# Kernel optimization log

Measured on AMD Instinct MI355X. Metric: run time of the kernel, lower is better.

## Reference

```python
import jax, jax.numpy as jnp
import numpy as np

HEADS = 16
DIM = 1024
D_K = DIM // HEADS
SEQ = 2048


def setup_inputs() -> dict:
    key = jax.random.key(0)
    ks = jax.random.split(key, 11)
    s = 1.0 / np.sqrt(DIM).astype(np.float32)
    return {
        "q": jax.random.normal(ks[0], (SEQ, DIM), jnp.float32),
        "k": jax.random.normal(ks[1], (SEQ, DIM), jnp.float32),
        "v": jax.random.normal(ks[2], (SEQ, DIM), jnp.float32),
        "Wq": jax.random.normal(ks[3], (DIM, DIM), jnp.float32) * s,
        "bq": jax.random.normal(ks[4], (DIM,), jnp.float32) * 0.01,
        "Wk": jax.random.normal(ks[5], (DIM, DIM), jnp.float32) * s,
        "bk": jax.random.normal(ks[6], (DIM,), jnp.float32) * 0.01,
        "Wv": jax.random.normal(ks[7], (DIM, DIM), jnp.float32) * s,
        "bv": jax.random.normal(ks[8], (DIM,), jnp.float32) * 0.01,
        "Wo": jax.random.normal(ks[9], (DIM, DIM), jnp.float32) * s,
        "bo": jax.random.normal(ks[10], (DIM,), jnp.float32) * 0.01,
    }


def reference(q, k, v, Wq, bq, Wk, bk, Wv, bv, Wo, bo):
    S = q.shape[0]
    # torch Linear: x @ W.T + b; view to (1, S, H, d_k) then transpose to (1, H, S, d_k)
    def proj(x, W, b):
        return (x @ W.T + b).reshape(1, S, HEADS, D_K).transpose(0, 2, 1, 3)

    qh = proj(q, Wq, bq)  # (1, H, S, d)
    kh = proj(k, Wk, bk)
    vh = proj(v, Wv, bv)

    scale = 1.0 / np.sqrt(D_K).astype(np.float32)
    scores = jnp.einsum("bhqd,bhkd->bhqk", qh, kh) * scale  # (1, H, S, S)
    # NOTE: source applies softmax over dim=1 == the HEADS axis (faithful quirk)
    attn = jax.nn.softmax(scores, axis=1)
    ctx = jnp.einsum("bhqk,bhkd->bhqd", attn, vh)  # (1, H, S, d)
    concat = ctx.transpose(0, 2, 1, 3).reshape(1, S, DIM)
    return concat @ Wo.T + bo
```

## Files before the change

kernel.cpp:

```cpp
#include <hip/hip_runtime.h>
#include <hip/hip_fp16.h>


typedef _Float16 f16;
typedef _Float16 f16x4 __attribute__((ext_vector_type(4)));
typedef _Float16 f16x8 __attribute__((ext_vector_type(8)));
typedef float    f32x4 __attribute__((ext_vector_type(4)));

#define S_LEN 2048
#define DIM   1024
#define NH    16
#define DK    64
#define EXP2K 0.1803368801111244f

#define MFMA(a, b, c) __builtin_amdgcn_mfma_f32_16x16x32_f16(a, b, c, 0, 0, 0)

#define VM_WAIT0   asm volatile("s_waitcnt vmcnt(0)" ::: "memory")
#define WG_BARRIER asm volatile("s_barrier" ::: "memory")

typedef __attribute__((address_space(1))) void g_void;
typedef __attribute__((address_space(3))) void l_void;

static __device__ __forceinline__ void gload_lds16(const void* g, void* l) {
  __builtin_amdgcn_global_load_lds((g_void*)g, (l_void*)l, 16, 0, 0);
}

static __device__ __forceinline__ float exp_s(float s) {
  return __builtin_amdgcn_exp2f(s * EXP2K);
}

__global__ __launch_bounds__(256) void cvt_all(
    const float* __restrict__ q, const float* __restrict__ k, const float* __restrict__ v,
    const float* __restrict__ Wq, const float* __restrict__ Wk, const float* __restrict__ Wv,
    const float* __restrict__ Wo, f16* __restrict__ qh, f16* __restrict__ kh,
    f16* __restrict__ vh, f16* __restrict__ wqh, f16* __restrict__ wkh,
    f16* __restrict__ wvh, f16* __restrict__ woh) {
  const size_t M = 1048576;
  const int seg = blockIdx.y;
  const float* src;
  f16* dst;
  switch (seg) {
    case 0: src = q;      dst = qh;      break;
    case 1: src = q + M;  dst = qh + M;  break;
    case 2: src = k;      dst = kh;      break;
    case 3: src = k + M;  dst = kh + M;  break;
    case 4: src = v;      dst = vh;      break;
    case 5: src = v + M;  dst = vh + M;  break;
    case 6: src = Wq;     dst = wqh;     break;
    case 7: src = Wk;     dst = wkh;     break;
    case 8: src = Wv;     dst = wvh;     break;
    default: src = Wo;    dst = woh;     break;
  }
  int i = blockIdx.x * 256 + threadIdx.x;
  float4 vv = ((const float4*)src)[i];
  f16x4 o = {(f16)vv.x, (f16)vv.y, (f16)vv.z, (f16)vv.w};
  ((f16x4*)dst)[i] = o;
}

__global__ __launch_bounds__(256) void cvt_f32_f16(const float* __restrict__ src,
                                                   f16* __restrict__ dst, int n4) {
  int i = blockIdx.x * 256 + threadIdx.x;
  if (i < n4) {
    float4 v = ((const float4*)src)[i];
    f16x4 o = {(f16)v.x, (f16)v.y, (f16)v.z, (f16)v.w};
    ((f16x4*)dst)[i] = o;
  }
}

static __device__ __forceinline__ void gemm32_core(const f16* __restrict__ X,
                                                   const f16* __restrict__ W,
                                                   int k0, int k1, int bm, int bn,
                                                   f16* As, f16* Bs,
                                                   f32x4 (&acc)[4][2]) {
  const int tid = threadIdx.x;
  const int wv = tid >> 6;
  const int lane = tid & 63;
  const int qd = lane >> 4;
  const int l16 = lane & 15;
  const int wm = (wv & 1) * 64;
  const int wn = (wv >> 1) * 32;
  const int lr4 = lane >> 2, lc4 = lane & 3;

  const f16* gA = X + (size_t)(bm + wv * 32 + lr4) * DIM + k0 + lc4 * 8;
  const f16* gB = W + (size_t)(bn + wv * 16 + lr4) * DIM + k0 + lc4 * 8;
  const int np = (k1 - k0) >> 5;

  gload_lds16(gA, As + (wv * 32) * 32);
  gload_lds16(gA + 16 * DIM, As + (wv * 32 + 16) * 32);
  gload_lds16(gB, Bs + (wv * 16) * 32);

#pragma unroll 2
  for (int t = 0; t < np; t++) {
    const int buf = t & 1;
    VM_WAIT0;
    WG_BARRIER;
    if (t + 1 < np) {
      const f16* gA1 = gA + (t + 1) * 32;
      const f16* gB1 = gB + (t + 1) * 32;
      f16* dA = As + (buf ^ 1) * (128 * 32);
      f16* dB = Bs + (buf ^ 1) * (64 * 32);
      gload_lds16(gA1, dA + (wv * 32) * 32);
      gload_lds16(gA1 + 16 * DIM, dA + (wv * 32 + 16) * 32);
      gload_lds16(gB1, dB + (wv * 16) * 32);
    }
    const f16* A = As + buf * (128 * 32);
    const f16* B = Bs + buf * (64 * 32);
    f16x8 bf[2];
#pragma unroll
    for (int ni = 0; ni < 2; ni++)
      bf[ni] = *(const f16x8*)&B[(wn + ni * 16 + l16) * 32 + qd * 8];
#pragma unroll
    for (int mi = 0; mi < 4; mi++) {
      f16x8 af = *(const f16x8*)&A[(wm + mi * 16 + l16) * 32 + qd * 8];
#pragma unroll
      for (int ni = 0; ni < 2; ni++)
        acc[mi][ni] = MFMA(af, bf[ni], acc[mi][ni]);
    }
  }
}

__global__ __launch_bounds__(256) void gemm_qkv(
    const f16* __restrict__ X0, const f16* __restrict__ X1, const f16* __restrict__ X2,
    const f16* __restrict__ W0, const f16* __restrict__ W1, const f16* __restrict__ W2,
    const float* __restrict__ b0, const float* __restrict__ b1, const float* __restrict__ b2,
    f16* __restrict__ o0, f16* __restrict__ o1, f16* __restrict__ o2) {
  __shared__ __align__(16) f16 As[2 * 128 * 32];
  __shared__ __align__(16) f16 Bs[2 * 64 * 32];
  const int z = blockIdx.z;
  const f16* X = z == 0 ? X0 : z == 1 ? X1 : X2;
  const f16* W = z == 0 ? W0 : z == 1 ? W1 : W2;
  const float* bias = z == 0 ? b0 : z == 1 ? b1 : b2;
  f16* outh = z == 0 ? o0 : z == 1 ? o1 : o2;

  const int bm = blockIdx.y * 128, bn = blockIdx.x * 64;
  f32x4 acc[4][2];
#pragma unroll
  for (int a = 0; a < 4; a++)
#pragma unroll
    for (int b = 0; b < 2; b++) acc[a][b] = (f32x4){0.f, 0.f, 0.f, 0.f};

  gemm32_core(X, W, 0, DIM, bm, bn, As, Bs, acc);

  const int tid = threadIdx.x;
  const int wv = tid >> 6, lane = tid & 63;
  const int qd = lane >> 4, l16 = lane & 15;
  const int wm = (wv & 1) * 64, wn = (wv >> 1) * 32;
#pragma unroll
  for (int mi = 0; mi < 4; mi++) {
#pragma unroll
    for (int ni = 0; ni < 2; ni++) {
      const int gm = bm + wm + mi * 16 + qd * 4;
      const int gn = bn + wn + ni * 16 + l16;
      const float bs = bias[gn];
      if (z == 2) {
        f16x4 o = {(f16)(acc[mi][ni][0] + bs), (f16)(acc[mi][ni][1] + bs),
                   (f16)(acc[mi][ni][2] + bs), (f16)(acc[mi][ni][3] + bs)};
        *(f16x4*)&outh[(size_t)gn * S_LEN + gm] = o;
      } else {
#pragma unroll
        for (int r = 0; r < 4; r++)
          outh[(size_t)(gm + r) * DIM + gn] = (f16)(acc[mi][ni][r] + bs);
      }
    }
  }
}

__global__ __launch_bounds__(256) void gemm_out(const f16* __restrict__ X,
                                                const f16* __restrict__ W,
                                                const float* __restrict__ bias,
                                                float* __restrict__ outf) {
  __shared__ __align__(16) f16 As[2 * 128 * 32];
  __shared__ __align__(16) f16 Bs[2 * 64 * 32];
  const int z = blockIdx.z;
  const int bm = blockIdx.y * 128, bn = blockIdx.x * 64;
  f32x4 acc[4][2];
#pragma unroll
  for (int a = 0; a < 4; a++)
#pragma unroll
    for (int b = 0; b < 2; b++) acc[a][b] = (f32x4){0.f, 0.f, 0.f, 0.f};

  gemm32_core(X, W, z * (DIM / 2), (z + 1) * (DIM / 2), bm, bn, As, Bs, acc);

  const int tid = threadIdx.x;
  const int wv = tid >> 6, lane = tid & 63;
  const int qd = lane >> 4, l16 = lane & 15;
  const int wm = (wv & 1) * 64, wn = (wv >> 1) * 32;
#pragma unroll
  for (int mi = 0; mi < 4; mi++) {
#pragma unroll
    for (int ni = 0; ni < 2; ni++) {
      const int gm = bm + wm + mi * 16 + qd * 4;
      const int gn = bn + wn + ni * 16 + l16;
      const float bs = z == 0 ? bias[gn] : 0.f;
#pragma unroll
      for (int r = 0; r < 4; r++)
        atomicAdd(&outf[(size_t)(gm + r) * DIM + gn], acc[mi][ni][r] + bs);
    }
  }
}

__global__ __launch_bounds__(256) void attn_denom(const f16* __restrict__ Qp,
                                                  const f16* __restrict__ Kp,
                                                  f16* __restrict__ IDn) {
  __shared__ __align__(16) f16 Qs[2][2][64 * 32];
  __shared__ __align__(16) f16 Ks[2][2][64 * 32];
  const int tid = threadIdx.x;
  const int wv = tid >> 6;
  const int lane = tid & 63;
  const int qd = lane >> 4;
  const int l16 = lane & 15;
  const int wm = (wv & 1) * 32, wn = (wv >> 1) * 32;
  const int bi = blockIdx.y * 64, bj = blockIdx.x * 64;
  const int lr4 = lane >> 2, lc4 = lane & 3;
  const int kkw = wv & 1;
  const int q0 = (wv >> 1) * 2;

  f32x4 dsum[2][2];
#pragma unroll
  for (int a = 0; a < 2; a++)
#pragma unroll
    for (int b = 0; b < 2; b++) dsum[a][b] = (f32x4){0.f, 0.f, 0.f, 0.f};

  {
    const f16* gq = Qp + (size_t)(bi + q0 * 16 + lr4) * DIM + kkw * 32 + lc4 * 8;
    const f16* gk = Kp + (size_t)(bj + q0 * 16 + lr4) * DIM + kkw * 32 + lc4 * 8;
#pragma unroll
    for (int t = 0; t < 2; t++) {
      gload_lds16(gq + (size_t)t * 16 * DIM, &Qs[0][kkw][(q0 + t) * 16 * 32]);
      gload_lds16(gk + (size_t)t * 16 * DIM, &Ks[0][kkw][(q0 + t) * 16 * 32]);
    }
  }

#pragma unroll 2
  for (int h = 0; h < NH; h++) {
    const int buf = h & 1;
    VM_WAIT0;
    WG_BARRIER;
    if (h + 1 < NH) {
      const f16* gq = Qp + (size_t)(bi + q0 * 16 + lr4) * DIM + (h + 1) * DK + kkw * 32 + lc4 * 8;
      const f16* gk = Kp + (size_t)(bj + q0 * 16 + lr4) * DIM + (h + 1) * DK + kkw * 32 + lc4 * 8;
#pragma unroll
      for (int t = 0; t < 2; t++) {
        gload_lds16(gq + (size_t)t * 16 * DIM, &Qs[buf ^ 1][kkw][(q0 + t) * 16 * 32]);
        gload_lds16(gk + (size_t)t * 16 * DIM, &Ks[buf ^ 1][kkw][(q0 + t) * 16 * 32]);
      }
    }

#pragma unroll
    for (int mi = 0; mi < 2; mi++) {
      f16x8 af0 = *(const f16x8*)&Qs[buf][0][(wm + mi * 16 + l16) * 32 + qd * 8];
      f16x8 af1 = *(const f16x8*)&Qs[buf][1][(wm + mi * 16 + l16) * 32 + qd * 8];
#pragma unroll
      for (int ni = 0; ni < 2; ni++) {
        f16x8 bf0 = *(const f16x8*)&Ks[buf][0][(wn + ni * 16 + l16) * 32 + qd * 8];
        f16x8 bf1 = *(const f16x8*)&Ks[buf][1][(wn + ni * 16 + l16) * 32 + qd * 8];
        f32x4 s = {0.f, 0.f, 0.f, 0.f};
        s = MFMA(af0, bf0, s);
        s = MFMA(af1, bf1, s);
#pragma unroll
        for (int r = 0; r < 4; r++) dsum[mi][ni][r] += exp_s(s[r]);
      }
    }
  }
#pragma unroll
  for (int mi = 0; mi < 2; mi++)
#pragma unroll
    for (int ni = 0; ni < 2; ni++)
#pragma unroll
      for (int r = 0; r < 4; r++) {
        const int gi = bi + wm + mi * 16 + qd * 4 + r;
        const int gj = bj + wn + ni * 16 + l16;
        IDn[(size_t)gi * S_LEN + gj] = (f16)(1.f / dsum[mi][ni][r]);
      }
}

__global__ __launch_bounds__(256, 4) void attn_ctx(const f16* __restrict__ Qp,
                                                   const f16* __restrict__ Kp,
                                                   const f16* __restrict__ Vt,
                                                   const f16* __restrict__ IDn,
                                                   float* __restrict__ Cp) {
  __shared__ __align__(16) f16 Ks[2][2][32 * 32];
  __shared__ __align__(16) f16 Vs[2][64 * 32];
  __shared__ __align__(16) f16 Pl[4][32 * 40];
  const int tid = threadIdx.x;
  const int wv = tid >> 6;
  const int lane = tid & 63;
  const int qd = lane >> 4;
  const int l16 = lane & 15;
  const int h = blockIdx.y;
  const int i0 = blockIdx.x * 128;
  const int iw = i0 + wv * 32;
  const int jb = blockIdx.z * 512;
  const int lr4 = lane >> 2, lc4 = lane & 3;
  const int kkw = wv & 1;
  const int rhw = wv >> 1;
  f16* pl = Pl[wv];

  f16x8 aq[2][2];
#pragma unroll
  for (int mi = 0; mi < 2; mi++)
#pragma unroll
    for (int kk = 0; kk < 2; kk++)
      aq[mi][kk] = *(const f16x8*)(Qp + (size_t)(iw + mi * 16 + l16) * DIM +
                                   h * DK + kk * 32 + qd * 8);

  f32x4 acc[2][4];
#pragma unroll
  for (int a = 0; a < 2; a++)
#pragma unroll
    for (int b = 0; b < 4; b++) acc[a][b] = (f32x4){0.f, 0.f, 0.f, 0.f};

  f16x8 idn[2][2];

  {
    const int j0 = jb;
    gload_lds16(Kp + (size_t)(j0 + rhw * 16 + lr4) * DIM + h * DK + kkw * 32 + lc4 * 8,
                &Ks[0][kkw][(rhw * 16) * 32]);
    gload_lds16(Vt + (size_t)(h * DK + wv * 16 + lr4) * S_LEN + j0 + lc4 * 8,
                &Vs[0][(wv * 16) * 32]);
#pragma unroll
    for (int mi = 0; mi < 2; mi++)
      idn[0][mi] = *(const f16x8*)(IDn + (size_t)(iw + mi * 16 + l16) * S_LEN + j0 + qd * 8);
  }

#pragma unroll 2
  for (int jt = 0; jt < 16; jt++) {
    const int buf = jt & 1;
    VM_WAIT0;
    WG_BARRIER;

    if (jt + 1 < 16) {
      const int j1 = jb + (jt + 1) * 32;
      gload_lds16(Kp + (size_t)(j1 + rhw * 16 + lr4) * DIM + h * DK + kkw * 32 + lc4 * 8,
                  &Ks[buf ^ 1][kkw][(rhw * 16) * 32]);
      gload_lds16(Vt + (size_t)(h * DK + wv * 16 + lr4) * S_LEN + j1 + lc4 * 8,
                  &Vs[buf ^ 1][(wv * 16) * 32]);
#pragma unroll
      for (int mi = 0; mi < 2; mi++)
        idn[buf ^ 1][mi] =
            *(const f16x8*)(IDn + (size_t)(iw + mi * 16 + l16) * S_LEN + j1 + qd * 8);
    }

    f16x8 bk[2][2];
#pragma unroll
    for (int ni = 0; ni < 2; ni++)
#pragma unroll
      for (int kk = 0; kk < 2; kk++)
        bk[ni][kk] = *(const f16x8*)&Ks[buf][kk][(ni * 16 + l16) * 32 + qd * 8];
#pragma unroll
    for (int mi = 0; mi < 2; mi++)
#pragma unroll
      for (int ni = 0; ni < 2; ni++) {
        f32x4 s = {0.f, 0.f, 0.f, 0.f};
        s = MFMA(aq[mi][0], bk[ni][0], s);
        s = MFMA(aq[mi][1], bk[ni][1], s);
#pragma unroll
        for (int r = 0; r < 4; r++)
          pl[(mi * 16 + qd * 4 + r) * 40 + ni * 16 + l16] = (f16)exp_s(s[r]);
      }

    f16x8 bv[4];
#pragma unroll
    for (int nd = 0; nd < 4; nd++)
      bv[nd] = *(const f16x8*)&Vs[buf][(nd * 16 + l16) * 32 + qd * 8];
#pragma unroll
    for (int mi = 0; mi < 2; mi++) {
      f16x8 ef = *(const f16x8*)&pl[(mi * 16 + l16) * 40 + qd * 8];
      f16x8 p = ef * idn[buf][mi];
#pragma unroll
      for (int nd = 0; nd < 4; nd++)
        acc[mi][nd] = MFMA(p, bv[nd], acc[mi][nd]);
    }
  }

#pragma unroll
  for (int mi = 0; mi < 2; mi++)
#pragma unroll
    for (int nd = 0; nd < 4; nd++)
#pragma unroll
      for (int r = 0; r < 4; r++)
        atomicAdd(&Cp[(size_t)(iw + mi * 16 + qd * 4 + r) * DIM + h * DK + nd * 16 + l16],
                  acc[mi][nd][r]);
}

extern "C" void kernel_launch(void* const* d_in, const int* in_sizes, int n_in,
                              void* d_out, int out_size, void* d_ws, size_t ws_size,
                              hipStream_t stream) {
  const float* q  = (const float*)d_in[0];
  const float* k  = (const float*)d_in[1];
  const float* v  = (const float*)d_in[2];
  const float* Wq = (const float*)d_in[3];
  const float* bq = (const float*)d_in[4];
  const float* Wk = (const float*)d_in[5];
  const float* bk = (const float*)d_in[6];
  const float* Wv = (const float*)d_in[7];
  const float* bv = (const float*)d_in[8];
  const float* Wo = (const float*)d_in[9];
  const float* bo = (const float*)d_in[10];
  float* out = (float*)d_out;

  f16* w = (f16*)d_ws;
  f16* qh  = w;
  f16* kh  = qh + (size_t)S_LEN * DIM;
  f16* vh  = kh + (size_t)S_LEN * DIM;
  f16* wqh = vh + (size_t)S_LEN * DIM;
  f16* wkh = wqh + (size_t)DIM * DIM;
  f16* wvh = wkh + (size_t)DIM * DIM;
  f16* woh = wvh + (size_t)DIM * DIM;
  f16* Qp  = woh + (size_t)DIM * DIM;
  f16* Kp  = Qp + (size_t)S_LEN * DIM;
  f16* Vt  = Kp + (size_t)S_LEN * DIM;
  f16* IDn = qh;
  float* Cp = (float*)vh;
  f16* Ct  = qh;

  dim3 b256(256);
  cvt_all<<<dim3(1024, 10), b256, 0, stream>>>(q, k, v, Wq, Wk, Wv, Wo,
                                               qh, kh, vh, wqh, wkh, wvh, woh);

  gemm_qkv<<<dim3(DIM / 64, S_LEN / 128, 3), b256, 0, stream>>>(
      qh, kh, vh, wqh, wkh, wvh, bq, bk, bv, Qp, Kp, Vt);

  hipMemsetAsync(Cp, 0, (size_t)S_LEN * DIM * sizeof(float), stream);
  hipMemsetAsync(out, 0, (size_t)S_LEN * DIM * sizeof(float), stream);

  attn_denom<<<dim3(S_LEN / 64, S_LEN / 64), b256, 0, stream>>>(Qp, Kp, IDn);
  attn_ctx<<<dim3(S_LEN / 128, NH, 4), b256, 0, stream>>>(Qp, Kp, Vt, IDn, Cp);

  const int nqkv4 = S_LEN * DIM / 4;
  cvt_f32_f16<<<nqkv4 / 256, b256, 0, stream>>>(Cp, Ct, nqkv4);

  gemm_out<<<dim3(DIM / 64, S_LEN / 128, 2), b256, 0, stream>>>(Ct, woh, bo, out);
}
```

Baseline: 229.3 us.

## Keep softmax probabilities in registers via transposed MFMA, swizzle V in LDS, split keys 8 ways

The attention-context kernel now computes scores with swapped MFMA operands (K as A, Q as B), so each lane's score outputs already sit in the A-operand layout for the P·V MFMA. This removes the per-wave LDS round trip for the exp'd probabilities, and the Pl shared buffer is dropped. V tiles are loaded into LDS with an XOR swizzle and read back as two f16x4 halves, aiming to cut bank conflicts. The key range per block is halved and the grid z doubled, with launch bounds raised to 5. The cost is more fp32 atomicAdd traffic into Cp and more blocks.

```diff
diff --git a/kernel.cpp b/kernel.cpp
--- a/kernel.cpp
+++ b/kernel.cpp
@@ -274,14 +274,13 @@
       }
 }
 
-__global__ __launch_bounds__(256, 4) void attn_ctx(const f16* __restrict__ Qp,
+__global__ __launch_bounds__(256, 5) void attn_ctx(const f16* __restrict__ Qp,
                                                    const f16* __restrict__ Kp,
                                                    const f16* __restrict__ Vt,
                                                    const f16* __restrict__ IDn,
                                                    float* __restrict__ Cp) {
   __shared__ __align__(16) f16 Ks[2][2][32 * 32];
   __shared__ __align__(16) f16 Vs[2][64 * 32];
-  __shared__ __align__(16) f16 Pl[4][32 * 40];
   const int tid = threadIdx.x;
   const int wv = tid >> 6;
   const int lane = tid & 63;
@@ -290,11 +289,10 @@
   const int h = blockIdx.y;
   const int i0 = blockIdx.x * 128;
   const int iw = i0 + wv * 32;
-  const int jb = blockIdx.z * 512;
+  const int jb = blockIdx.z * 256;
   const int lr4 = lane >> 2, lc4 = lane & 3;
   const int kkw = wv & 1;
   const int rhw = wv >> 1;
-  f16* pl = Pl[wv];
 
   f16x8 aq[2][2];
 #pragma unroll
@@ -310,35 +308,43 @@
 #pragma unroll
     for (int b = 0; b < 4; b++) acc[a][b] = (f32x4){0.f, 0.f, 0.f, 0.f};
 
-  f16x8 idn[2][2];
+  f16x4 idn[2][2][2];
+
+  const int vswz = (lc4 ^ ((lr4 >> 1) & 3)) * 8;
 
   {
     const int j0 = jb;
     gload_lds16(Kp + (size_t)(j0 + rhw * 16 + lr4) * DIM + h * DK + kkw * 32 + lc4 * 8,
                 &Ks[0][kkw][(rhw * 16) * 32]);
-    gload_lds16(Vt + (size_t)(h * DK + wv * 16 + lr4) * S_LEN + j0 + lc4 * 8,
+    gload_lds16(Vt + (size_t)(h * DK + wv * 16 + lr4) * S_LEN + j0 + vswz,
                 &Vs[0][(wv * 16) * 32]);
 #pragma unroll
     for (int mi = 0; mi < 2; mi++)
-      idn[0][mi] = *(const f16x8*)(IDn + (size_t)(iw + mi * 16 + l16) * S_LEN + j0 + qd * 8);
+#pragma unroll
+      for (int ni = 0; ni < 2; ni++)
+        idn[0][mi][ni] = *(const f16x4*)(IDn + (size_t)(iw + mi * 16 + l16) * S_LEN +
+                                         j0 + ni * 16 + qd * 4);
   }
 
 #pragma unroll 2
-  for (int jt = 0; jt < 16; jt++) {
+  for (int jt = 0; jt < 8; jt++) {
     const int buf = jt & 1;
     VM_WAIT0;
     WG_BARRIER;
 
-    if (jt + 1 < 16) {
+    if (jt + 1 < 8) {
       const int j1 = jb + (jt + 1) * 32;
       gload_lds16(Kp + (size_t)(j1 + rhw * 16 + lr4) * DIM + h * DK + kkw * 32 + lc4 * 8,
                   &Ks[buf ^ 1][kkw][(rhw * 16) * 32]);
-      gload_lds16(Vt + (size_t)(h * DK + wv * 16 + lr4) * S_LEN + j1 + lc4 * 8,
+      gload_lds16(Vt + (size_t)(h * DK + wv * 16 + lr4) * S_LEN + j1 + vswz,
                   &Vs[buf ^ 1][(wv * 16) * 32]);
 #pragma unroll
       for (int mi = 0; mi < 2; mi++)
-        idn[buf ^ 1][mi] =
-            *(const f16x8*)(IDn + (size_t)(iw + mi * 16 + l16) * S_LEN + j1 + qd * 8);
+#pragma unroll
+        for (int ni = 0; ni < 2; ni++)
+          idn[buf ^ 1][mi][ni] =
+              *(const f16x4*)(IDn + (size_t)(iw + mi * 16 + l16) * S_LEN +
+                              j1 + ni * 16 + qd * 4);
     }
 
     f16x8 bk[2][2];
@@ -347,30 +353,43 @@
 #pragma unroll
       for (int kk = 0; kk < 2; kk++)
         bk[ni][kk] = *(const f16x8*)&Ks[buf][kk][(ni * 16 + l16) * 32 + qd * 8];
+
+    f16x8 pa[2];
+#pragma unroll
+    for (int mi = 0; mi < 2; mi++) {
+      f32x4 st0 = {0.f, 0.f, 0.f, 0.f};
+      f32x4 st1 = {0.f, 0.f, 0.f, 0.f};
+      st0 = MFMA(bk[0][0], aq[mi][0], st0);
+      st0 = MFMA(bk[0][1], aq[mi][1], st0);
+      st1 = MFMA(bk[1][0], aq[mi][0], st1);
+      st1 = MFMA(bk[1][1], aq[mi][1], st1);
+      const f16x4 i0v = idn[buf][mi][0];
+      const f16x4 i1v = idn[buf][mi][1];
+      f16x8 p;
+#pragma unroll
+      for (int r = 0; r < 4; r++) p[r] = (f16)(exp_s(st0[r]) * (float)i0v[r]);
+#pragma unroll
+      for (int r = 0; r < 4; r++) p[4 + r] = (f16)(exp_s(st1[r]) * (float)i1v[r]);
+      pa[mi] = p;
+    }
+
+    const int xsw = (l16 >> 1) & 3;
+    const int q04 = (qd & 1) * 4;
+    const int sq = qd >> 1;
+    f16x8 bv[4];
+#pragma unroll
+    for (int nd = 0; nd < 4; nd++) {
+      const f16* vb = &Vs[buf][(nd * 16 + l16) * 32];
+      f16x4 lo = *(const f16x4*)&vb[((sq ^ xsw) * 8) + q04];
+      f16x4 hi = *(const f16x4*)&vb[(((2 + sq) ^ xsw) * 8) + q04];
+      bv[nd] = __builtin_shufflevector(lo, hi, 0, 1, 2, 3, 4, 5, 6, 7);
+    }
+
 #pragma unroll
     for (int mi = 0; mi < 2; mi++)
 #pragma unroll
-      for (int ni = 0; ni < 2; ni++) {
-        f32x4 s = {0.f, 0.f, 0.f, 0.f};
-        s = MFMA(aq[mi][0], bk[ni][0], s);
-        s = MFMA(aq[mi][1], bk[ni][1], s);
-#pragma unroll
-        for (int r = 0; r < 4; r++)
-          pl[(mi * 16 + qd * 4 + r) * 40 + ni * 16 + l16] = (f16)exp_s(s[r]);
-      }
-
-    f16x8 bv[4];
-#pragma unroll
-    for (int nd = 0; nd < 4; nd++)
-      bv[nd] = *(const f16x8*)&Vs[buf][(nd * 16 + l16) * 32 + qd * 8];
-#pragma unroll
-    for (int mi = 0; mi < 2; mi++) {
-      f16x8 ef = *(const f16x8*)&pl[(mi * 16 + l16) * 40 + qd * 8];
-      f16x8 p = ef * idn[buf][mi];
-#pragma unroll
       for (int nd = 0; nd < 4; nd++)
-        acc[mi][nd] = MFMA(p, bv[nd], acc[mi][nd]);
-    }
+        acc[mi][nd] = MFMA(pa[mi], bv[nd], acc[mi][nd]);
   }
 
 #pragma unroll
@@ -425,7 +444,7 @@
   hipMemsetAsync(out, 0, (size_t)S_LEN * DIM * sizeof(float), stream);
 
   attn_denom<<<dim3(S_LEN / 64, S_LEN / 64), b256, 0, stream>>>(Qp, Kp, IDn);
-  attn_ctx<<<dim3(S_LEN / 128, NH, 4), b256, 0, stream>>>(Qp, Kp, Vt, IDn, Cp);
+  attn_ctx<<<dim3(S_LEN / 128, NH, 8), b256, 0, stream>>>(Qp, Kp, Vt, IDn, Cp);
 
   const int nqkv4 = S_LEN * DIM / 4;
   cvt_f32_f16<<<nqkv4 / 256, b256, 0, stream>>>(Cp, Ct, nqkv4);
```

Result: slower. 277.3 us (+20.9%).

## Keep softmax probabilities in registers and triple-buffer 64-wide K/V tiles in attn_ctx

Applied to the files above, without the earlier changes.

The attention-context kernel now computes S^T via swapped MFMA operands, so each lane's exp scores already sit in the layout the PV MFMA needs as its A operand. This removes the per-wave LDS round trip for P. The key tile grows from 32 to 64 columns with a three-stage buffer and a partial vmcnt wait, so more loads stay in flight. The V-transpose projection output is stored in a permuted column order, and V tiles are loaded into LDS with an XOR swizzle to avoid bank conflicts. In exchange the kernel uses more LDS and registers, and occupancy hints drop from 4 to 3 blocks per CU.

```diff
diff --git a/kernel.cpp b/kernel.cpp
--- a/kernel.cpp
+++ b/kernel.cpp
@@ -16,6 +16,7 @@
 #define MFMA(a, b, c) __builtin_amdgcn_mfma_f32_16x16x32_f16(a, b, c, 0, 0, 0)
 
 #define VM_WAIT0   asm volatile("s_waitcnt vmcnt(0)" ::: "memory")
+#define VM_WAIT12  asm volatile("s_waitcnt vmcnt(12)" ::: "memory")
 #define WG_BARRIER asm volatile("s_barrier" ::: "memory")
 
 typedef __attribute__((address_space(1))) void g_void;
@@ -155,7 +156,8 @@
       if (z == 2) {
         f16x4 o = {(f16)(acc[mi][ni][0] + bs), (f16)(acc[mi][ni][1] + bs),
                    (f16)(acc[mi][ni][2] + bs), (f16)(acc[mi][ni][3] + bs)};
-        *(f16x4*)&outh[(size_t)gn * S_LEN + gm] = o;
+        const int pj = (gm & ~31) + ((gm >> 2) & 3) * 8 + ((gm >> 4) & 1) * 4;
+        *(f16x4*)&outh[(size_t)gn * S_LEN + pj] = o;
       } else {
 #pragma unroll
         for (int r = 0; r < 4; r++)
@@ -274,27 +276,25 @@
       }
 }
 
-__global__ __launch_bounds__(256, 4) void attn_ctx(const f16* __restrict__ Qp,
+__global__ __launch_bounds__(256, 3) void attn_ctx(const f16* __restrict__ Qp,
                                                    const f16* __restrict__ Kp,
                                                    const f16* __restrict__ Vt,
                                                    const f16* __restrict__ IDn,
                                                    float* __restrict__ Cp) {
-  __shared__ __align__(16) f16 Ks[2][2][32 * 32];
-  __shared__ __align__(16) f16 Vs[2][64 * 32];
-  __shared__ __align__(16) f16 Pl[4][32 * 40];
+  __shared__ __align__(16) f16 Ks[3][2][64 * 32];
+  __shared__ __align__(16) f16 Vs[3][64 * 64];
   const int tid = threadIdx.x;
   const int wv = tid >> 6;
   const int lane = tid & 63;
   const int qd = lane >> 4;
   const int l16 = lane & 15;
   const int h = blockIdx.y;
-  const int i0 = blockIdx.x * 128;
-  const int iw = i0 + wv * 32;
+  const int iw = blockIdx.x * 128 + wv * 32;
   const int jb = blockIdx.z * 512;
   const int lr4 = lane >> 2, lc4 = lane & 3;
+  const int lr8 = lane >> 3, lc8 = lane & 7;
   const int kkw = wv & 1;
   const int rhw = wv >> 1;
-  f16* pl = Pl[wv];
 
   f16x8 aq[2][2];
 #pragma unroll
@@ -310,66 +310,77 @@
 #pragma unroll
     for (int b = 0; b < 4; b++) acc[a][b] = (f32x4){0.f, 0.f, 0.f, 0.f};
 
-  f16x8 idn[2][2];
-
-  {
-    const int j0 = jb;
-    gload_lds16(Kp + (size_t)(j0 + rhw * 16 + lr4) * DIM + h * DK + kkw * 32 + lc4 * 8,
-                &Ks[0][kkw][(rhw * 16) * 32]);
-    gload_lds16(Vt + (size_t)(h * DK + wv * 16 + lr4) * S_LEN + j0 + lc4 * 8,
-                &Vs[0][(wv * 16) * 32]);
+  f16x4 idn[3][2][4];
+
+  auto issue = [&](int tt, int pb) {
+    const int j1 = jb + tt * 64;
+    const f16* gk = Kp + (size_t)(j1 + rhw * 16 + lr4) * DIM + h * DK + kkw * 32 + lc4 * 8;
+    gload_lds16(gk, &Ks[pb][kkw][(rhw * 16) * 32]);
+    gload_lds16(gk + (size_t)32 * DIM, &Ks[pb][kkw][(rhw * 16 + 32) * 32]);
+    const f16* gv = Vt + (size_t)(h * DK + wv * 8 + lr8) * S_LEN + j1 + (lc8 ^ lr8) * 8;
+    gload_lds16(gv, &Vs[pb][(wv * 8) * 64]);
+    gload_lds16(gv + (size_t)32 * S_LEN, &Vs[pb][(wv * 8 + 32) * 64]);
 #pragma unroll
     for (int mi = 0; mi < 2; mi++)
-      idn[0][mi] = *(const f16x8*)(IDn + (size_t)(iw + mi * 16 + l16) * S_LEN + j0 + qd * 8);
-  }
-
-#pragma unroll 2
-  for (int jt = 0; jt < 16; jt++) {
-    const int buf = jt & 1;
-    VM_WAIT0;
+#pragma unroll
+      for (int ni = 0; ni < 4; ni++)
+        idn[pb][mi][ni] = *(const f16x4*)(IDn + (size_t)(iw + mi * 16 + l16) * S_LEN +
+                                          j1 + ni * 16 + qd * 4);
+  };
+
+  issue(0, 0);
+  issue(1, 1);
+
+#pragma unroll
+  for (int t = 0; t < 8; t++) {
+    const int buf = t % 3;
+    if (t == 7) { VM_WAIT0; } else { VM_WAIT12; }
     WG_BARRIER;
-
-    if (jt + 1 < 16) {
-      const int j1 = jb + (jt + 1) * 32;
-      gload_lds16(Kp + (size_t)(j1 + rhw * 16 + lr4) * DIM + h * DK + kkw * 32 + lc4 * 8,
-                  &Ks[buf ^ 1][kkw][(rhw * 16) * 32]);
-      gload_lds16(Vt + (size_t)(h * DK + wv * 16 + lr4) * S_LEN + j1 + lc4 * 8,
-                  &Vs[buf ^ 1][(wv * 16) * 32]);
-#pragma unroll
-      for (int mi = 0; mi < 2; mi++)
-        idn[buf ^ 1][mi] =
-            *(const f16x8*)(IDn + (size_t)(iw + mi * 16 + l16) * S_LEN + j1 + qd * 8);
-    }
-
-    f16x8 bk[2][2];
-#pragma unroll
-    for (int ni = 0; ni < 2; ni++)
+    if (t + 2 < 8) issue(t + 2, (t + 2) % 3);
+
+    f16x8 bk[4][2];
+#pragma unroll
+    for (int ni = 0; ni < 4; ni++)
 #pragma unroll
       for (int kk = 0; kk < 2; kk++)
         bk[ni][kk] = *(const f16x8*)&Ks[buf][kk][(ni * 16 + l16) * 32 + qd * 8];
-#pragma unroll
-    for (int mi = 0; mi < 2; mi++)
-#pragma unroll
-      for (int ni = 0; ni < 2; ni++) {
+
+    f16x8 pa[2][2];
+#pragma unroll
+    for (int mi = 0; mi < 2; mi++) {
+      f32x4 st[4];
+#pragma unroll
+      for (int ni = 0; ni < 4; ni++) {
         f32x4 s = {0.f, 0.f, 0.f, 0.f};
-        s = MFMA(aq[mi][0], bk[ni][0], s);
-        s = MFMA(aq[mi][1], bk[ni][1], s);
+        s = MFMA(bk[ni][0], aq[mi][0], s);
+        s = MFMA(bk[ni][1], aq[mi][1], s);
+        st[ni] = s;
+      }
+#pragma unroll
+      for (int js = 0; js < 2; js++) {
+        f16x8 p;
 #pragma unroll
         for (int r = 0; r < 4; r++)
-          pl[(mi * 16 + qd * 4 + r) * 40 + ni * 16 + l16] = (f16)exp_s(s[r]);
-      }
-
-    f16x8 bv[4];
-#pragma unroll
-    for (int nd = 0; nd < 4; nd++)
-      bv[nd] = *(const f16x8*)&Vs[buf][(nd * 16 + l16) * 32 + qd * 8];
-#pragma unroll
-    for (int mi = 0; mi < 2; mi++) {
-      f16x8 ef = *(const f16x8*)&pl[(mi * 16 + l16) * 40 + qd * 8];
-      f16x8 p = ef * idn[buf][mi];
+          p[r] = (f16)(exp_s(st[js * 2][r]) * (float)idn[buf][mi][js * 2][r]);
+#pragma unroll
+        for (int r = 0; r < 4; r++)
+          p[4 + r] = (f16)(exp_s(st[js * 2 + 1][r]) * (float)idn[buf][mi][js * 2 + 1][r]);
+        pa[mi][js] = p;
+      }
+    }
+
+#pragma unroll
+    for (int js = 0; js < 2; js++) {
+      f16x8 bv[4];
 #pragma unroll
       for (int nd = 0; nd < 4; nd++)
-        acc[mi][nd] = MFMA(p, bv[nd], acc[mi][nd]);
+        bv[nd] = *(const f16x8*)&Vs[buf][(nd * 16 + l16) * 64 +
+                                        (((js * 4 + qd) ^ (l16 & 7)) * 8)];
+#pragma unroll
+      for (int mi = 0; mi < 2; mi++)
+#pragma unroll
+        for (int nd = 0; nd < 4; nd++)
+          acc[mi][nd] = MFMA(pa[mi][js], bv[nd], acc[mi][nd]);
     }
   }
 
```

Result: no change. 231.1 us (+0.8%).

## Keep attention probabilities in registers via transposed MFMA and permuted V layout

Applied to the files above, without the earlier changes.

The context kernel now computes the score tile as K·Q^T so the MFMA output lands in the register layout the P·V MFMA needs as its A operand. This removes the per-wave LDS round trip for P. The V projection epilogue writes V^T with its sequence index permuted to match that register layout. The kernel also drops LDS staging and barriers for K and V and reads them straight from global memory (cache) per wave. The trade-off is redundant global/L2 traffic across the four waves with no double buffering to hide load latency.

```diff
diff --git a/kernel.cpp b/kernel.cpp
--- a/kernel.cpp
+++ b/kernel.cpp
@@ -155,7 +155,8 @@
       if (z == 2) {
         f16x4 o = {(f16)(acc[mi][ni][0] + bs), (f16)(acc[mi][ni][1] + bs),
                    (f16)(acc[mi][ni][2] + bs), (f16)(acc[mi][ni][3] + bs)};
-        *(f16x4*)&outh[(size_t)gn * S_LEN + gm] = o;
+        const int pj = (gm & ~31) + ((gm >> 2) & 3) * 8 + ((gm >> 4) & 1) * 4;
+        *(f16x4*)&outh[(size_t)gn * S_LEN + pj] = o;
       } else {
 #pragma unroll
         for (int r = 0; r < 4; r++)
@@ -279,22 +280,14 @@
                                                    const f16* __restrict__ Vt,
                                                    const f16* __restrict__ IDn,
                                                    float* __restrict__ Cp) {
-  __shared__ __align__(16) f16 Ks[2][2][32 * 32];
-  __shared__ __align__(16) f16 Vs[2][64 * 32];
-  __shared__ __align__(16) f16 Pl[4][32 * 40];
   const int tid = threadIdx.x;
   const int wv = tid >> 6;
   const int lane = tid & 63;
   const int qd = lane >> 4;
   const int l16 = lane & 15;
   const int h = blockIdx.y;
-  const int i0 = blockIdx.x * 128;
-  const int iw = i0 + wv * 32;
+  const int iw = blockIdx.x * 128 + wv * 32;
   const int jb = blockIdx.z * 512;
-  const int lr4 = lane >> 2, lc4 = lane & 3;
-  const int kkw = wv & 1;
-  const int rhw = wv >> 1;
-  f16* pl = Pl[wv];
 
   f16x8 aq[2][2];
 #pragma unroll
@@ -310,67 +303,54 @@
 #pragma unroll
     for (int b = 0; b < 4; b++) acc[a][b] = (f32x4){0.f, 0.f, 0.f, 0.f};
 
-  f16x8 idn[2][2];
-
-  {
-    const int j0 = jb;
-    gload_lds16(Kp + (size_t)(j0 + rhw * 16 + lr4) * DIM + h * DK + kkw * 32 + lc4 * 8,
-                &Ks[0][kkw][(rhw * 16) * 32]);
-    gload_lds16(Vt + (size_t)(h * DK + wv * 16 + lr4) * S_LEN + j0 + lc4 * 8,
-                &Vs[0][(wv * 16) * 32]);
+  const f16* kp = Kp + (size_t)(jb + l16) * DIM + h * DK + qd * 8;
+  const f16* vp = Vt + (size_t)(h * DK + l16) * S_LEN + jb + qd * 8;
+  const f16* ip = IDn + (size_t)(iw + l16) * S_LEN + jb + qd * 4;
+
+#pragma unroll 2
+  for (int t = 0; t < 16; t++) {
+    const int j0 = t * 32;
+    f16x8 bk[2][2];
+#pragma unroll
+    for (int ni = 0; ni < 2; ni++)
+#pragma unroll
+      for (int kk = 0; kk < 2; kk++)
+        bk[ni][kk] = *(const f16x8*)(kp + (size_t)(j0 + ni * 16) * DIM + kk * 32);
+    f16x8 bv[4];
+#pragma unroll
+    for (int nd = 0; nd < 4; nd++)
+      bv[nd] = *(const f16x8*)(vp + (size_t)(nd * 16) * S_LEN + j0);
+    f16x4 idn[2][2];
 #pragma unroll
     for (int mi = 0; mi < 2; mi++)
-      idn[0][mi] = *(const f16x8*)(IDn + (size_t)(iw + mi * 16 + l16) * S_LEN + j0 + qd * 8);
-  }
-
-#pragma unroll 2
-  for (int jt = 0; jt < 16; jt++) {
-    const int buf = jt & 1;
-    VM_WAIT0;
-    WG_BARRIER;
-
-    if (jt + 1 < 16) {
-      const int j1 = jb + (jt + 1) * 32;
-      gload_lds16(Kp + (size_t)(j1 + rhw * 16 + lr4) * DIM + h * DK + kkw * 32 + lc4 * 8,
-                  &Ks[buf ^ 1][kkw][(rhw * 16) * 32]);
-      gload_lds16(Vt + (size_t)(h * DK + wv * 16 + lr4) * S_LEN + j1 + lc4 * 8,
-                  &Vs[buf ^ 1][(wv * 16) * 32]);
-#pragma unroll
-      for (int mi = 0; mi < 2; mi++)
-        idn[buf ^ 1][mi] =
-            *(const f16x8*)(IDn + (size_t)(iw + mi * 16 + l16) * S_LEN + j1 + qd * 8);
-    }
-
-    f16x8 bk[2][2];
-#pragma unroll
-    for (int ni = 0; ni < 2; ni++)
-#pragma unroll
-      for (int kk = 0; kk < 2; kk++)
-        bk[ni][kk] = *(const f16x8*)&Ks[buf][kk][(ni * 16 + l16) * 32 + qd * 8];
+#pragma unroll
+      for (int ni = 0; ni < 2; ni++)
+        idn[mi][ni] = *(const f16x4*)(ip + (size_t)(mi * 16) * S_LEN + j0 + ni * 16);
+
+    f16x8 pa[2];
+#pragma unroll
+    for (int mi = 0; mi < 2; mi++) {
+      f32x4 st0 = {0.f, 0.f, 0.f, 0.f};
+      f32x4 st1 = {0.f, 0.f, 0.f, 0.f};
+      st0 = MFMA(bk[0][0], aq[mi][0], st0);
+      st0 = MFMA(bk[0][1], aq[mi][1], st0);
+      st1 = MFMA(bk[1][0], aq[mi][0], st1);
+      st1 = MFMA(bk[1][1], aq[mi][1], st1);
+      f16x8 p;
+#pragma unroll
+      for (int r = 0; r < 4; r++)
+        p[r] = (f16)(exp_s(st0[r]) * (float)idn[mi][0][r]);
+#pragma unroll
+      for (int r = 0; r < 4; r++)
+        p[4 + r] = (f16)(exp_s(st1[r]) * (float)idn[mi][1][r]);
+      pa[mi] = p;
+    }
+
 #pragma unroll
     for (int mi = 0; mi < 2; mi++)
 #pragma unroll
-      for (int ni = 0; ni < 2; ni++) {
-        f32x4 s = {0.f, 0.f, 0.f, 0.f};
-        s = MFMA(aq[mi][0], bk[ni][0], s);
-        s = MFMA(aq[mi][1], bk[ni][1], s);
-#pragma unroll
-        for (int r = 0; r < 4; r++)
-          pl[(mi * 16 + qd * 4 + r) * 40 + ni * 16 + l16] = (f16)exp_s(s[r]);
-      }
-
-    f16x8 bv[4];
-#pragma unroll
-    for (int nd = 0; nd < 4; nd++)
-      bv[nd] = *(const f16x8*)&Vs[buf][(nd * 16 + l16) * 32 + qd * 8];
-#pragma unroll
-    for (int mi = 0; mi < 2; mi++) {
-      f16x8 ef = *(const f16x8*)&pl[(mi * 16 + l16) * 40 + qd * 8];
-      f16x8 p = ef * idn[buf][mi];
-#pragma unroll
       for (int nd = 0; nd < 4; nd++)
-        acc[mi][nd] = MFMA(p, bv[nd], acc[mi][nd]);
-    }
+        acc[mi][nd] = MFMA(pa[mi], bv[nd], acc[mi][nd]);
   }
 
 #pragma unroll
```

After: 287.4 us. 25.3% more time.
